# Kernel optimization log

Measured on AMD Instinct MI355X. Metric: run time of the kernel, lower is better.

Reference implementation:

```python
import jax, jax.numpy as jnp
import numpy as np

# ---- constants derived exactly as in CQCCExtractor.__init__ ----
SR = 16000
FMIN = 32.7
N_BINS = 96
BINS_OCT = 24
N_CQCC = 20
HOP = 128
Q = 1.0 / (2.0 ** (1.0 / BINS_OCT) - 1.0)
MIN_WIN = max(16, int(Q * SR / FMIN))          # 16699
N_FFT = 1
while N_FFT < MIN_WIN * 2:
    N_FFT <<= 1                                # 65536
NUM_FREQ = N_FFT // 2 + 1                      # 32769


def _dct_mat():
    k = np.arange(N_CQCC)[:, None]
    n = np.arange(N_BINS)[None, :]
    return jnp.asarray(np.cos(np.pi * k * (2 * n + 1) / (2 * N_BINS)), dtype=jnp.float32)


def _delta(feat, N=2):
    # vectorized version of the per-frame python loop: d[t] = sum_n n*(f[min(t+n,T-1)] - f[max(t-n,0)]) / denom
    denom = 2 * sum(i * i for i in range(1, N + 1))
    T = feat.shape[0]
    p = jnp.concatenate([jnp.repeat(feat[:1], N, axis=0), feat, jnp.repeat(feat[-1:], N, axis=0)], axis=0)
    num = sum(n * (p[N + n:N + n + T] - p[N - n:N - n + T]) for n in range(1, N + 1))
    return num / denom


def setup_inputs() -> dict:
    key = jax.random.key(0)
    wav = jax.random.normal(key, (262144,), dtype=jnp.float32)
    return {"wav": wav}


def reference(wav) -> jnp.ndarray:
    # periodic hann window of length MIN_WIN, zero-padded (centered) to N_FFT like torch.stft
    w = 0.5 - 0.5 * jnp.cos(2.0 * jnp.pi * jnp.arange(MIN_WIN, dtype=jnp.float32) / MIN_WIN)
    left = (N_FFT - MIN_WIN) // 2
    win = jnp.zeros((N_FFT,), dtype=jnp.float32).at[left:left + MIN_WIN].set(w)

    # torch.stft(center=True, pad_mode='reflect')
    pad = N_FFT // 2
    x = jnp.pad(wav, pad, mode='reflect')
    n_frames = 1 + wav.shape[0] // HOP
    starts = jnp.arange(n_frames) * HOP
    frames = x[starts[:, None] + jnp.arange(N_FFT)[None, :]] * win      # [T, n_fft]
    spec = jnp.fft.rfft(frames, axis=-1)                                 # [T, F] complex64
    power = jnp.abs(spec) ** 2                                           # [T, F]

    # linear interpolation of STFT power at geometrically spaced CQT freqs
    cqt_freqs = FMIN * 2.0 ** (jnp.arange(N_BINS, dtype=jnp.float32) / BINS_OCT)
    idx_float = cqt_freqs / (SR / 2) * (NUM_FREQ - 1)
    idx_lo = jnp.clip(idx_float.astype(jnp.int32), 0, NUM_FREQ - 2)
    idx_hi = idx_lo + 1
    alpha = (idx_float - idx_lo.astype(jnp.float32))                     # [n_bins]
    cqt_power = (1.0 - alpha) * power[:, idx_lo] + alpha * power[:, idx_hi]  # [T, n_bins]

    log_cqt = jnp.log(jnp.maximum(cqt_power, 1e-8))
    cqcc = log_cqt @ _dct_mat().T                                        # [T, n_cqcc]
    # normalize over time (torch.std default is unbiased, ddof=1)
    cqcc = (cqcc - cqcc.mean(axis=0)) / (jnp.std(cqcc, axis=0, ddof=1) + 1e-8)

    d1 = _delta(cqcc)
    d2 = _delta(d1)
    return jnp.concatenate([cqcc, d1, d2], axis=-1)                      # [T, 3*n_cqcc]
```

## Files before the change

### kernel.cpp

```cpp
#include <hip/hip_runtime.h>
#include <math.h>

#define WAV_N     262144
#define HOP       128
#define MIN_WIN   16699
#define LEFT      24418
#define T_FRAMES  2049
#define N_BINS    96
#define N_CQCC    20
#define F_COMP    192
#define NF        576
#define NBLK      2179
#define NBP       2240
#define PARTLEN   59
#define FULLBLK   130
#define XS_VALID  278843
#define TWOPI     6.283185307179586f

#define BT   64
#define FTW  32
#define JC   32
#define AST  68

#define WS_QFP  0
#define WS_SC   20643840
#define WS_CQ   23801856
#define WS_SUMS 23965776
#define SCP     2056

__device__ __forceinline__ void f_to_fi_sigma(int f, int& fi, int& sigma) {
    int plane = f / 192;
    int c = f - plane * 192;
    int bin = c >> 1, hi = c & 1;
    float e    = (float)bin / 24.0f;
    float fb   = 32.7f * exp2f(e);
    float idxf = fb / 8000.0f * 32768.0f;
    fi = (int)idxf + hi;
    sigma = (plane == 0) ? 0 : (plane == 1 ? 1 : -1);
}

__global__ __launch_bounds__(256) void k_chunk(const float* __restrict__ wav,
                                               float4* __restrict__ QFP) {
    __shared__ float A_lds[JC * AST];
    int tid = threadIdx.x;
    int b0 = blockIdx.x * BT;
    int f0 = blockIdx.y * FTW;
    int ftp = tid & 15;
    int bg  = tid >> 4;
    int bb  = b0 + bg * 4;

    int fi[2], sg[2];
    f_to_fi_sigma(f0 + 2 * ftp,     fi[0], sg[0]);
    f_to_fi_sigma(f0 + 2 * ftp + 1, fi[1], sg[1]);

    float Dr[2], Di[2];
    #pragma unroll
    for (int h = 0; h < 2; ++h) {
        float fr = (float)fi[h] * (1.0f / 65536.0f)
                 - (float)sg[h] * (1.0f / (float)MIN_WIN);
        fr -= rintf(fr);
        float sn, cs; __sincosf(TWOPI * fr, &sn, &cs);
        Dr[h] = cs; Di[h] = -sn;
    }

    float xr[2][4], xi[2][4], pr[2][4], pi[2][4];
    #pragma unroll
    for (int h = 0; h < 2; ++h)
        #pragma unroll
        for (int i = 0; i < 4; ++i) { xr[h][i] = 0.f; xi[h][i] = 0.f; }

    for (int jc = 0; jc < 4; ++jc) {
        int jbase = jc * JC;
        __syncthreads();
        #pragma unroll
        for (int i = 0; i < 8; ++i) {
            int m = i * 256 + tid;
            int j = m & 31, bl = m >> 5;
            int s = 128 * (b0 + bl) + jbase + j;
            float v = 0.0f;
            if (s < XS_VALID) {
                int w = s - 8350;
                if (w < 0) w = -w;
                if (w >= WAV_N) w = 2 * WAV_N - 2 - w;
                v = wav[w];
            }
            A_lds[j * AST + bl] = v;
        }
        __syncthreads();
        float Wr[2], Wi[2];
        #pragma unroll
        for (int h = 0; h < 2; ++h) {
            float fr = (float)((jbase * fi[h]) & 65535) * (1.0f / 65536.0f)
                     - (float)sg[h] * (float)jbase * (1.0f / (float)MIN_WIN);
            fr -= rintf(fr);
            float sn, cs; __sincosf(TWOPI * fr, &sn, &cs);
            Wr[h] = cs; Wi[h] = -sn;
        }
        #pragma unroll 8
        for (int j32 = 0; j32 < JC; ++j32) {
            if (jc == 1 && j32 == PARTLEN - 32) {
                #pragma unroll
                for (int h = 0; h < 2; ++h)
                    #pragma unroll
                    for (int i = 0; i < 4; ++i) { pr[h][i] = xr[h][i]; pi[h][i] = xi[h][i]; }
            }
            float4 a = *(const float4*)&A_lds[j32 * AST + bg * 4];
            const float aa[4] = {a.x, a.y, a.z, a.w};
            #pragma unroll
            for (int h = 0; h < 2; ++h) {
                float wr = Wr[h], wi = Wi[h];
                #pragma unroll
                for (int i = 0; i < 4; ++i) {
                    xr[h][i] = fmaf(aa[i], wr, xr[h][i]);
                    xi[h][i] = fmaf(aa[i], wi, xi[h][i]);
                }
                Wr[h] = wr * Dr[h] - wi * Di[h];
                Wi[h] = wr * Di[h] + wi * Dr[h];
            }
        }
    }

    #pragma unroll
    for (int h = 0; h < 2; ++h) {
        int f = f0 + 2 * ftp + h;
        float4* dst = QFP + (size_t)f * NBP + bb;
        #pragma unroll
        for (int i = 0; i < 4; ++i) {
            int b = bb + i;
            unsigned ph = ((unsigned)fi[h] * (unsigned)(LEFT + 128 * b)) & 65535u;
            float frf = (float)ph * (1.0f / 65536.0f)
                      - (float)sg[h] * (float)((128 * b) % MIN_WIN) * (1.0f / (float)MIN_WIN);
            frf -= rintf(frf);
            float sn, cs; __sincosf(TWOPI * frf, &sn, &cs);
            dst[i] = make_float4(xr[h][i] * cs + xi[h][i] * sn,
                                 xi[h][i] * cs - xr[h][i] * sn,
                                 pr[h][i] * cs + pi[h][i] * sn,
                                 pi[h][i] * cs - pr[h][i] * sn);
        }
    }
}

#define SEG 9
__global__ __launch_bounds__(256) void k_scan(const float4* __restrict__ QFP,
                                              float2* __restrict__ Sc,
                                              double* __restrict__ sums) {
    __shared__ float4 col[NBLK];
    __shared__ float2 acc[T_FRAMES];
    __shared__ double2 wsum[4];
    int tid = threadIdx.x;
    int c = blockIdx.x;
    if (c == 0 && tid < 40) sums[tid] = 0.0;

    for (int plane = 0; plane < 3; ++plane) {
        int f = plane * 192 + c;
        const float4* g = QFP + (size_t)f * NBP;
        #pragma unroll
        for (int k = 0; k < SEG; ++k) {
            int idx = k * 256 + tid;
            if (idx < NBLK) col[idx] = g[idx];
        }
        __syncthreads();
        int s0 = tid * SEG, s1 = min(s0 + SEG, NBLK);
        double sr = 0.0, si = 0.0;
        for (int i = s0; i < s1; ++i) { sr += col[i].x; si += col[i].y; }
        double r = sr, im = si;
        #pragma unroll
        for (int off = 1; off < 64; off <<= 1) {
            double prx = __shfl_up(r, off);
            double piy = __shfl_up(im, off);
            if ((tid & 63) >= off) { r += prx; im += piy; }
        }
        if ((tid & 63) == 63) wsum[tid >> 6] = make_double2(r, im);
        __syncthreads();
        double basr = 0.0, basi = 0.0;
        int w = tid >> 6;
        for (int ww = 0; ww < w; ++ww) { basr += wsum[ww].x; basi += wsum[ww].y; }
        double gr = basr + r - sr, gi = basi + im - si;
        for (int i = s0; i < s1; ++i) {
            float qx = col[i].x, qy = col[i].y;
            col[i].x = (float)gr; col[i].y = (float)gi;
            gr += qx; gi += qy;
        }
        __syncthreads();
        int fi_, sg_; f_to_fi_sigma(f, fi_, sg_);
        #pragma unroll
        for (int k = 0; k < SEG; ++k) {
            int t = k * 256 + tid;
            if (t < T_FRAMES) {
                float4 ca = col[t];
                float4 cb = col[t + FULLBLK];
                float ur = cb.x - ca.x + cb.z;
                float ui = cb.y - ca.y + cb.w;
                unsigned ph = ((unsigned)fi_ * 128u * (unsigned)t) & 65535u;
                float frf = (float)ph * (1.0f / 65536.0f)
                          - (float)sg_ * (float)((128 * t) % MIN_WIN) * (1.0f / (float)MIN_WIN);
                frf -= rintf(frf);
                float sn, cs;
                __sincosf(TWOPI * frf, &sn, &cs);
                float vr = ur * cs - ui * sn;
                float vi = ur * sn + ui * cs;
                if (plane == 0) acc[t] = make_float2(0.5f * vr, 0.5f * vi);
                else { acc[t].x -= 0.25f * vr; acc[t].y -= 0.25f * vi; }
            }
        }
        __syncthreads();
    }
    #pragma unroll
    for (int k = 0; k < SEG; ++k) {
        int t = k * 256 + tid;
        if (t < T_FRAMES) Sc[(size_t)c * SCP + t] = acc[t];
    }
}

__global__ __launch_bounds__(256) void k_cqt(const float2* __restrict__ Sc,
                                             float* __restrict__ cq,
                                             double* __restrict__ sums) {
    __shared__ float dctm[N_CQCC * N_BINS];
    __shared__ float lg[8][N_BINS];
    __shared__ float cqv[8][N_CQCC];
    int tid = threadIdx.x;
    int tb = blockIdx.x * 8;
    for (int idx = tid; idx < N_CQCC * N_BINS; idx += 256) {
        int k = idx / N_BINS, b = idx - k * N_BINS;
        dctm[idx] = cosf((float)M_PI * (float)(k * (2 * b + 1)) / 192.0f);
    }
    int lt = tid >> 5, lane = tid & 31;
    int t = tb + lt;
    #pragma unroll
    for (int bb = 0; bb < 3; ++bb) {
        int b = lane + 32 * bb;
        float lv = 0.0f;
        if (t < T_FRAMES) {
            float2 lo = Sc[(size_t)(2 * b) * SCP + t];
            float2 hi = Sc[(size_t)(2 * b + 1) * SCP + t];
            float pl = lo.x * lo.x + lo.y * lo.y;
            float ph = hi.x * hi.x + hi.y * hi.y;
            float e    = (float)b / 24.0f;
            float fb   = 32.7f * exp2f(e);
            float idxf = fb / 8000.0f * 32768.0f;
            float alpha = idxf - (float)((int)idxf);
            float p = (1.0f - alpha) * pl + alpha * ph;
            lv = logf(fmaxf(p, 1e-8f));
        }
        lg[lt][b] = lv;
    }
    __syncthreads();
    if (tid < 8 * N_CQCC) {
        int lt2 = tid / N_CQCC, k = tid - lt2 * N_CQCC;
        int t2 = tb + lt2;
        float s = 0.0f;
        #pragma unroll 4
        for (int b = 0; b < N_BINS; ++b) s += dctm[k * N_BINS + b] * lg[lt2][b];
        cqv[lt2][k] = (t2 < T_FRAMES) ? s : 0.0f;
        if (t2 < T_FRAMES) cq[t2 * N_CQCC + k] = s;
    }
    __syncthreads();
    if (tid < N_CQCC) {
        double s1 = 0.0, s2 = 0.0;
        #pragma unroll
        for (int lt2 = 0; lt2 < 8; ++lt2) {
            if (tb + lt2 < T_FRAMES) {
                double v = (double)cqv[lt2][tid];
                s1 += v; s2 += v * v;
            }
        }
        atomicAdd(&sums[tid], s1);
        atomicAdd(&sums[N_CQCC + tid], s2);
    }
}

__device__ __forceinline__ int clampT(int v) {
    return v < 0 ? 0 : (v > T_FRAMES - 1 ? T_FRAMES - 1 : v);
}

__global__ void k_final(const float* __restrict__ cq, const double* __restrict__ sums,
                        float* __restrict__ out) {
    int gid = blockIdx.x * blockDim.x + threadIdx.x;
    if (gid >= T_FRAMES * N_CQCC) return;
    int t = gid / N_CQCC;
    int k = gid - t * N_CQCC;
    double S1 = sums[k], S2 = sums[N_CQCC + k];
    double md = S1 / (double)T_FRAMES;
    double var = (S2 - S1 * md) / (double)(T_FRAMES - 1);
    double sd = sqrt(var > 0.0 ? var : 0.0);
    float m = (float)md;
    float iv = (float)(1.0 / (sd + 1e-8));
    float cv[9];
    #pragma unroll
    for (int j = 0; j < 9; ++j)
        cv[j] = (cq[clampT(t + j - 4) * N_CQCC + k] - m) * iv;
    float dv[5];
    #pragma unroll
    for (int o = -2; o <= 2; ++o) {
        int p = clampT(t + o);
        int h1 = clampT(p + 1) - t, l1 = clampT(p - 1) - t;
        int h2 = clampT(p + 2) - t, l2 = clampT(p - 2) - t;
        dv[o + 2] = ((cv[h1 + 4] - cv[l1 + 4]) + 2.0f * (cv[h2 + 4] - cv[l2 + 4])) * 0.1f;
    }
    out[t * 60 + k]      = cv[4];
    out[t * 60 + 20 + k] = dv[2];
    out[t * 60 + 40 + k] = (dv[3] - dv[1] + 2.0f * (dv[4] - dv[0])) * 0.1f;
}

extern "C" void kernel_launch(void* const* d_in, const int* in_sizes, int n_in,
                              void* d_out, int out_size, void* d_ws, size_t ws_size,
                              hipStream_t stream) {
    const float* wav = (const float*)d_in[0];
    float* out = (float*)d_out;
    char* ws = (char*)d_ws;
    float4* QFP  = (float4*)(ws + WS_QFP);
    float2* Sc   = (float2*)(ws + WS_SC);
    float*  cq   = (float*)(ws + WS_CQ);
    double* sums = (double*)(ws + WS_SUMS);

    k_chunk<<<dim3(NBP / BT, NF / FTW), 256, 0, stream>>>(wav, QFP);
    k_scan<<<F_COMP, 256, 0, stream>>>(QFP, Sc, sums);
    k_cqt<<<(T_FRAMES + 7) / 8, 256, 0, stream>>>(Sc, cq, sums);
    k_final<<<(T_FRAMES * N_CQCC + 255) / 256, 256, 0, stream>>>(cq, sums, out);
}
```

Measured before the change: 117.5 us.

## Split scan per frequency plane across blocks and move plane combine to cqt

The scan kernel previously ran 192 blocks, each walking the three frequency planes in sequence. It now launches 576 blocks, one per plane-frequency, so more of the GPU's compute units have work. To allow that, the chunk kernel writes the full-block and partial-block sums into two separate float2 arrays instead of one float4 array. The scan reads the partial sums straight from global memory and writes per-frequency results in time-major order. The 0.5/-0.25 plane combine moves into the cqt kernel, which now reads contiguous rows. In exchange, the scan's stores are strided by 576 elements and are uncoalesced, and more intermediate data passes through global memory.

```diff
diff --git a/kernel.cpp b/kernel.cpp
--- a/kernel.cpp
+++ b/kernel.cpp
@@ -22,11 +22,11 @@
 #define JC   32
 #define AST  68
 
-#define WS_QFP  0
-#define WS_SC   20643840
-#define WS_CQ   23801856
-#define WS_SUMS 23965776
-#define SCP     2056
+#define WS_QF   0
+#define WS_QP   10321920
+#define WS_VT   20643840
+#define WS_CQ   30085632
+#define WS_SUMS 30249552
 
 __device__ __forceinline__ void f_to_fi_sigma(int f, int& fi, int& sigma) {
     int plane = f / 192;
@@ -40,7 +40,8 @@
 }
 
 __global__ __launch_bounds__(256) void k_chunk(const float* __restrict__ wav,
-                                               float4* __restrict__ QFP) {
+                                               float2* __restrict__ QF,
+                                               float2* __restrict__ QP) {
     __shared__ float A_lds[JC * AST];
     int tid = threadIdx.x;
     int b0 = blockIdx.x * BT;
@@ -123,7 +124,8 @@
     #pragma unroll
     for (int h = 0; h < 2; ++h) {
         int f = f0 + 2 * ftp + h;
-        float4* dst = QFP + (size_t)f * NBP + bb;
+        float2* dstF = QF + (size_t)f * NBP + bb;
+        float2* dstP = QP + (size_t)f * NBP + bb;
         #pragma unroll
         for (int i = 0; i < 4; ++i) {
             int b = bb + i;
@@ -132,90 +134,81 @@
                       - (float)sg[h] * (float)((128 * b) % MIN_WIN) * (1.0f / (float)MIN_WIN);
             frf -= rintf(frf);
             float sn, cs; __sincosf(TWOPI * frf, &sn, &cs);
-            dst[i] = make_float4(xr[h][i] * cs + xi[h][i] * sn,
-                                 xi[h][i] * cs - xr[h][i] * sn,
-                                 pr[h][i] * cs + pi[h][i] * sn,
-                                 pi[h][i] * cs - pr[h][i] * sn);
+            dstF[i] = make_float2(xr[h][i] * cs + xi[h][i] * sn,
+                                  xi[h][i] * cs - xr[h][i] * sn);
+            dstP[i] = make_float2(pr[h][i] * cs + pi[h][i] * sn,
+                                  pi[h][i] * cs - pr[h][i] * sn);
         }
     }
 }
 
 #define SEG 9
-__global__ __launch_bounds__(256) void k_scan(const float4* __restrict__ QFP,
-                                              float2* __restrict__ Sc,
+__global__ __launch_bounds__(256) void k_scan(const float2* __restrict__ QF,
+                                              const float2* __restrict__ QP,
+                                              float2* __restrict__ VT,
                                               double* __restrict__ sums) {
-    __shared__ float4 col[NBLK];
-    __shared__ float2 acc[T_FRAMES];
+    __shared__ float2 col[NBLK];
     __shared__ double2 wsum[4];
     int tid = threadIdx.x;
-    int c = blockIdx.x;
-    if (c == 0 && tid < 40) sums[tid] = 0.0;
-
-    for (int plane = 0; plane < 3; ++plane) {
-        int f = plane * 192 + c;
-        const float4* g = QFP + (size_t)f * NBP;
-        #pragma unroll
-        for (int k = 0; k < SEG; ++k) {
-            int idx = k * 256 + tid;
-            if (idx < NBLK) col[idx] = g[idx];
-        }
-        __syncthreads();
-        int s0 = tid * SEG, s1 = min(s0 + SEG, NBLK);
-        double sr = 0.0, si = 0.0;
-        for (int i = s0; i < s1; ++i) { sr += col[i].x; si += col[i].y; }
-        double r = sr, im = si;
-        #pragma unroll
-        for (int off = 1; off < 64; off <<= 1) {
-            double prx = __shfl_up(r, off);
-            double piy = __shfl_up(im, off);
-            if ((tid & 63) >= off) { r += prx; im += piy; }
-        }
-        if ((tid & 63) == 63) wsum[tid >> 6] = make_double2(r, im);
-        __syncthreads();
-        double basr = 0.0, basi = 0.0;
-        int w = tid >> 6;
-        for (int ww = 0; ww < w; ++ww) { basr += wsum[ww].x; basi += wsum[ww].y; }
-        double gr = basr + r - sr, gi = basi + im - si;
-        for (int i = s0; i < s1; ++i) {
-            float qx = col[i].x, qy = col[i].y;
-            col[i].x = (float)gr; col[i].y = (float)gi;
-            gr += qx; gi += qy;
-        }
-        __syncthreads();
-        int fi_, sg_; f_to_fi_sigma(f, fi_, sg_);
-        #pragma unroll
-        for (int k = 0; k < SEG; ++k) {
-            int t = k * 256 + tid;
-            if (t < T_FRAMES) {
-                float4 ca = col[t];
-                float4 cb = col[t + FULLBLK];
-                float ur = cb.x - ca.x + cb.z;
-                float ui = cb.y - ca.y + cb.w;
-                unsigned ph = ((unsigned)fi_ * 128u * (unsigned)t) & 65535u;
-                float frf = (float)ph * (1.0f / 65536.0f)
-                          - (float)sg_ * (float)((128 * t) % MIN_WIN) * (1.0f / (float)MIN_WIN);
-                frf -= rintf(frf);
-                float sn, cs;
-                __sincosf(TWOPI * frf, &sn, &cs);
-                float vr = ur * cs - ui * sn;
-                float vi = ur * sn + ui * cs;
-                if (plane == 0) acc[t] = make_float2(0.5f * vr, 0.5f * vi);
-                else { acc[t].x -= 0.25f * vr; acc[t].y -= 0.25f * vi; }
-            }
-        }
-        __syncthreads();
-    }
+    int f = blockIdx.x;
+    if (f == 0 && tid < 40) sums[tid] = 0.0;
+
+    const float2* g = QF + (size_t)f * NBP;
+    #pragma unroll
+    for (int k = 0; k < SEG; ++k) {
+        int idx = k * 256 + tid;
+        if (idx < NBLK) col[idx] = g[idx];
+    }
+    __syncthreads();
+    int s0 = tid * SEG, s1 = min(s0 + SEG, NBLK);
+    double sr = 0.0, si = 0.0;
+    for (int i = s0; i < s1; ++i) { sr += col[i].x; si += col[i].y; }
+    double r = sr, im = si;
+    #pragma unroll
+    for (int off = 1; off < 64; off <<= 1) {
+        double prx = __shfl_up(r, off);
+        double piy = __shfl_up(im, off);
+        if ((tid & 63) >= off) { r += prx; im += piy; }
+    }
+    if ((tid & 63) == 63) wsum[tid >> 6] = make_double2(r, im);
+    __syncthreads();
+    double basr = 0.0, basi = 0.0;
+    int w = tid >> 6;
+    for (int ww = 0; ww < w; ++ww) { basr += wsum[ww].x; basi += wsum[ww].y; }
+    double gr = basr + r - sr, gi = basi + im - si;
+    for (int i = s0; i < s1; ++i) {
+        float qx = col[i].x, qy = col[i].y;
+        col[i].x = (float)gr; col[i].y = (float)gi;
+        gr += qx; gi += qy;
+    }
+    __syncthreads();
+    int fi_, sg_; f_to_fi_sigma(f, fi_, sg_);
     #pragma unroll
     for (int k = 0; k < SEG; ++k) {
         int t = k * 256 + tid;
-        if (t < T_FRAMES) Sc[(size_t)c * SCP + t] = acc[t];
-    }
-}
-
-__global__ __launch_bounds__(256) void k_cqt(const float2* __restrict__ Sc,
+        if (t < T_FRAMES) {
+            float2 g0 = col[t];
+            float2 g1 = col[t + FULLBLK];
+            float2 qp = QP[(size_t)f * NBP + t + FULLBLK];
+            float ur = g1.x - g0.x + qp.x;
+            float ui = g1.y - g0.y + qp.y;
+            unsigned ph = ((unsigned)fi_ * 128u * (unsigned)t) & 65535u;
+            float frf = (float)ph * (1.0f / 65536.0f)
+                      - (float)sg_ * (float)((128 * t) % MIN_WIN) * (1.0f / (float)MIN_WIN);
+            frf -= rintf(frf);
+            float sn, cs;
+            __sincosf(TWOPI * frf, &sn, &cs);
+            VT[(size_t)t * NF + f] = make_float2(ur * cs - ui * sn,
+                                                 ur * sn + ui * cs);
+        }
+    }
+}
+
+__global__ __launch_bounds__(256) void k_cqt(const float2* __restrict__ VT,
                                              float* __restrict__ cq,
                                              double* __restrict__ sums) {
     __shared__ float dctm[N_CQCC * N_BINS];
+    __shared__ float2 sc[8][F_COMP];
     __shared__ float lg[8][N_BINS];
     __shared__ float cqv[8][N_CQCC];
     int tid = threadIdx.x;
@@ -224,43 +217,48 @@
         int k = idx / N_BINS, b = idx - k * N_BINS;
         dctm[idx] = cosf((float)M_PI * (float)(k * (2 * b + 1)) / 192.0f);
     }
-    int lt = tid >> 5, lane = tid & 31;
-    int t = tb + lt;
-    #pragma unroll
-    for (int bb = 0; bb < 3; ++bb) {
-        int b = lane + 32 * bb;
-        float lv = 0.0f;
+    for (int idx = tid; idx < 8 * F_COMP; idx += 256) {
+        int lt = idx / F_COMP, c = idx - lt * F_COMP;
+        int t = tb + lt;
+        float2 v = make_float2(0.f, 0.f);
         if (t < T_FRAMES) {
-            float2 lo = Sc[(size_t)(2 * b) * SCP + t];
-            float2 hi = Sc[(size_t)(2 * b + 1) * SCP + t];
-            float pl = lo.x * lo.x + lo.y * lo.y;
-            float ph = hi.x * hi.x + hi.y * hi.y;
-            float e    = (float)b / 24.0f;
-            float fb   = 32.7f * exp2f(e);
-            float idxf = fb / 8000.0f * 32768.0f;
-            float alpha = idxf - (float)((int)idxf);
-            float p = (1.0f - alpha) * pl + alpha * ph;
-            lv = logf(fmaxf(p, 1e-8f));
-        }
-        lg[lt][b] = lv;
+            const float2* row = VT + (size_t)t * NF;
+            float2 v0 = row[c], v1 = row[192 + c], v2 = row[384 + c];
+            v = make_float2(0.5f * v0.x - 0.25f * (v1.x + v2.x),
+                            0.5f * v0.y - 0.25f * (v1.y + v2.y));
+        }
+        sc[lt][c] = v;
+    }
+    __syncthreads();
+    for (int idx = tid; idx < 8 * N_BINS; idx += 256) {
+        int lt = idx / N_BINS, b = idx - lt * N_BINS;
+        float2 lo = sc[lt][2 * b], hi = sc[lt][2 * b + 1];
+        float pl = lo.x * lo.x + lo.y * lo.y;
+        float ph = hi.x * hi.x + hi.y * hi.y;
+        float e    = (float)b / 24.0f;
+        float fb   = 32.7f * exp2f(e);
+        float idxf = fb / 8000.0f * 32768.0f;
+        float alpha = idxf - (float)((int)idxf);
+        float p = (1.0f - alpha) * pl + alpha * ph;
+        lg[lt][b] = logf(fmaxf(p, 1e-8f));
     }
     __syncthreads();
     if (tid < 8 * N_CQCC) {
-        int lt2 = tid / N_CQCC, k = tid - lt2 * N_CQCC;
-        int t2 = tb + lt2;
+        int lt = tid / N_CQCC, k = tid - lt * N_CQCC;
+        int t = tb + lt;
         float s = 0.0f;
         #pragma unroll 4
-        for (int b = 0; b < N_BINS; ++b) s += dctm[k * N_BINS + b] * lg[lt2][b];
-        cqv[lt2][k] = (t2 < T_FRAMES) ? s : 0.0f;
-        if (t2 < T_FRAMES) cq[t2 * N_CQCC + k] = s;
+        for (int b = 0; b < N_BINS; ++b) s += dctm[k * N_BINS + b] * lg[lt][b];
+        cqv[lt][k] = (t < T_FRAMES) ? s : 0.0f;
+        if (t < T_FRAMES) cq[t * N_CQCC + k] = s;
     }
     __syncthreads();
     if (tid < N_CQCC) {
         double s1 = 0.0, s2 = 0.0;
         #pragma unroll
-        for (int lt2 = 0; lt2 < 8; ++lt2) {
-            if (tb + lt2 < T_FRAMES) {
-                double v = (double)cqv[lt2][tid];
+        for (int lt = 0; lt < 8; ++lt) {
+            if (tb + lt < T_FRAMES) {
+                double v = (double)cqv[lt][tid];
                 s1 += v; s2 += v * v;
             }
         }
@@ -308,13 +306,14 @@
     const float* wav = (const float*)d_in[0];
     float* out = (float*)d_out;
     char* ws = (char*)d_ws;
-    float4* QFP  = (float4*)(ws + WS_QFP);
-    float2* Sc   = (float2*)(ws + WS_SC);
+    float2* QF   = (float2*)(ws + WS_QF);
+    float2* QP   = (float2*)(ws + WS_QP);
+    float2* VT   = (float2*)(ws + WS_VT);
     float*  cq   = (float*)(ws + WS_CQ);
     double* sums = (double*)(ws + WS_SUMS);
 
-    k_chunk<<<dim3(NBP / BT, NF / FTW), 256, 0, stream>>>(wav, QFP);
-    k_scan<<<F_COMP, 256, 0, stream>>>(QFP, Sc, sums);
-    k_cqt<<<(T_FRAMES + 7) / 8, 256, 0, stream>>>(Sc, cq, sums);
+    k_chunk<<<dim3(NBP / BT, NF / FTW), 256, 0, stream>>>(wav, QF, QP);
+    k_scan<<<NF, 256, 0, stream>>>(QF, QP, VT, sums);
+    k_cqt<<<(T_FRAMES + 7) / 8, 256, 0, stream>>>(VT, cq, sums);
     k_final<<<(T_FRAMES * N_CQCC + 255) / 256, 256, 0, stream>>>(cq, sums, out);
 }
```

Result: slower. 122.1 us (+4.0%).

## Process all three planes of k_scan concurrently with one shared-memory pass

Applied to the files above, without the earlier changes.

k_scan now loads the prefix-sum columns for all three frequency planes at once and keeps only the float2 part in shared memory. It runs the three scans together, which cuts the number of block barriers and raises independent work per thread. The second float2 of each float4 is no longer staged in LDS and is read directly from global memory in the output phase. The per-frame accumulator array is replaced by register accumulation. The trade is about 52KB of LDS, more registers for the triple double-precision scan, and uncoalesced strided global reads of the .zw halves.

```diff
diff --git a/kernel.cpp b/kernel.cpp
--- a/kernel.cpp
+++ b/kernel.cpp
@@ -144,71 +144,97 @@
 __global__ __launch_bounds__(256) void k_scan(const float4* __restrict__ QFP,
                                               float2* __restrict__ Sc,
                                               double* __restrict__ sums) {
-    __shared__ float4 col[NBLK];
-    __shared__ float2 acc[T_FRAMES];
-    __shared__ double2 wsum[4];
+    __shared__ float2 col[3 * NBLK];
+    __shared__ double2 wsum[3][4];
     int tid = threadIdx.x;
     int c = blockIdx.x;
     if (c == 0 && tid < 40) sums[tid] = 0.0;
 
-    for (int plane = 0; plane < 3; ++plane) {
-        int f = plane * 192 + c;
-        const float4* g = QFP + (size_t)f * NBP;
+    const float2* base = (const float2*)QFP;
+    #pragma unroll
+    for (int p = 0; p < 3; ++p) {
+        size_t foff = (size_t)(p * 192 + c) * NBP;
         #pragma unroll
         for (int k = 0; k < SEG; ++k) {
             int idx = k * 256 + tid;
-            if (idx < NBLK) col[idx] = g[idx];
-        }
-        __syncthreads();
-        int s0 = tid * SEG, s1 = min(s0 + SEG, NBLK);
-        double sr = 0.0, si = 0.0;
-        for (int i = s0; i < s1; ++i) { sr += col[i].x; si += col[i].y; }
-        double r = sr, im = si;
-        #pragma unroll
-        for (int off = 1; off < 64; off <<= 1) {
-            double prx = __shfl_up(r, off);
-            double piy = __shfl_up(im, off);
-            if ((tid & 63) >= off) { r += prx; im += piy; }
-        }
-        if ((tid & 63) == 63) wsum[tid >> 6] = make_double2(r, im);
-        __syncthreads();
+            if (idx < NBLK) col[p * NBLK + idx] = base[2 * (foff + idx)];
+        }
+    }
+    __syncthreads();
+
+    int s0 = tid * SEG, s1 = min(s0 + SEG, NBLK);
+    double sr[3] = {0, 0, 0}, si[3] = {0, 0, 0};
+    #pragma unroll
+    for (int p = 0; p < 3; ++p)
+        for (int i = s0; i < s1; ++i) {
+            sr[p] += col[p * NBLK + i].x;
+            si[p] += col[p * NBLK + i].y;
+        }
+    double r[3], im[3];
+    #pragma unroll
+    for (int p = 0; p < 3; ++p) { r[p] = sr[p]; im[p] = si[p]; }
+    #pragma unroll
+    for (int off = 1; off < 64; off <<= 1) {
+        #pragma unroll
+        for (int p = 0; p < 3; ++p) {
+            double prx = __shfl_up(r[p], off);
+            double piy = __shfl_up(im[p], off);
+            if ((tid & 63) >= off) { r[p] += prx; im[p] += piy; }
+        }
+    }
+    if ((tid & 63) == 63) {
+        #pragma unroll
+        for (int p = 0; p < 3; ++p) wsum[p][tid >> 6] = make_double2(r[p], im[p]);
+    }
+    __syncthreads();
+    int w = tid >> 6;
+    double gr[3], gi[3];
+    #pragma unroll
+    for (int p = 0; p < 3; ++p) {
         double basr = 0.0, basi = 0.0;
-        int w = tid >> 6;
-        for (int ww = 0; ww < w; ++ww) { basr += wsum[ww].x; basi += wsum[ww].y; }
-        double gr = basr + r - sr, gi = basi + im - si;
-        for (int i = s0; i < s1; ++i) {
-            float qx = col[i].x, qy = col[i].y;
-            col[i].x = (float)gr; col[i].y = (float)gi;
-            gr += qx; gi += qy;
-        }
-        __syncthreads();
-        int fi_, sg_; f_to_fi_sigma(f, fi_, sg_);
-        #pragma unroll
-        for (int k = 0; k < SEG; ++k) {
-            int t = k * 256 + tid;
-            if (t < T_FRAMES) {
-                float4 ca = col[t];
-                float4 cb = col[t + FULLBLK];
-                float ur = cb.x - ca.x + cb.z;
-                float ui = cb.y - ca.y + cb.w;
-                unsigned ph = ((unsigned)fi_ * 128u * (unsigned)t) & 65535u;
+        for (int ww = 0; ww < w; ++ww) { basr += wsum[p][ww].x; basi += wsum[p][ww].y; }
+        gr[p] = basr + r[p] - sr[p];
+        gi[p] = basi + im[p] - si[p];
+    }
+    for (int i = s0; i < s1; ++i) {
+        #pragma unroll
+        for (int p = 0; p < 3; ++p) {
+            float2 old = col[p * NBLK + i];
+            col[p * NBLK + i] = make_float2((float)gr[p], (float)gi[p]);
+            gr[p] += old.x; gi[p] += old.y;
+        }
+    }
+    __syncthreads();
+
+    int fi_[3], sg_[3];
+    #pragma unroll
+    for (int p = 0; p < 3; ++p) f_to_fi_sigma(p * 192 + c, fi_[p], sg_[p]);
+    #pragma unroll
+    for (int k = 0; k < SEG; ++k) {
+        int t = k * 256 + tid;
+        if (t < T_FRAMES) {
+            float accx = 0.0f, accy = 0.0f;
+            #pragma unroll
+            for (int p = 0; p < 3; ++p) {
+                float2 g0 = col[p * NBLK + t];
+                float2 g1 = col[p * NBLK + t + FULLBLK];
+                float2 qp = base[2 * ((size_t)(p * 192 + c) * NBP + t + FULLBLK) + 1];
+                float ur = g1.x - g0.x + qp.x;
+                float ui = g1.y - g0.y + qp.y;
+                unsigned ph = ((unsigned)fi_[p] * 128u * (unsigned)t) & 65535u;
                 float frf = (float)ph * (1.0f / 65536.0f)
-                          - (float)sg_ * (float)((128 * t) % MIN_WIN) * (1.0f / (float)MIN_WIN);
+                          - (float)sg_[p] * (float)((128 * t) % MIN_WIN) * (1.0f / (float)MIN_WIN);
                 frf -= rintf(frf);
                 float sn, cs;
                 __sincosf(TWOPI * frf, &sn, &cs);
                 float vr = ur * cs - ui * sn;
                 float vi = ur * sn + ui * cs;
-                if (plane == 0) acc[t] = make_float2(0.5f * vr, 0.5f * vi);
-                else { acc[t].x -= 0.25f * vr; acc[t].y -= 0.25f * vi; }
-            }
-        }
-        __syncthreads();
-    }
-    #pragma unroll
-    for (int k = 0; k < SEG; ++k) {
-        int t = k * 256 + tid;
-        if (t < T_FRAMES) Sc[(size_t)c * SCP + t] = acc[t];
+                float wgt = (p == 0) ? 0.5f : -0.25f;
+                accx = fmaf(wgt, vr, accx);
+                accy = fmaf(wgt, vi, accy);
+            }
+            Sc[(size_t)c * SCP + t] = make_float2(accx, accy);
+        }
     }
 }
 
```

Measured after the change: 114.8 us. 2.3% less time.
